# Performance work log

Hardware: AMD Instinct MI355X
Metric: run time of the kernel (lower is better)

## Reference

```python
import jax, jax.numpy as jnp
import numpy as np

ML, KS, L = 3, 7, 7  # mL, kernelSize, L = 2*mL+1


def _conv(img, kern, pad, groups=1):
    # img: [N,C,H,W], kern: [O, C//groups, kh, kw]
    return jax.lax.conv_general_dilated(
        img, kern, (1, 1), [(pad, pad), (pad, pad)],
        dimension_numbers=("NCHW", "OIHW", "NCHW"),
        feature_group_count=groups)


def setup_inputs() -> dict:
    key = jax.random.key(0)
    ks = jax.random.split(key, 16)
    B, MU = 64, 256
    lin = lambda k, fi, fo: (jax.random.normal(k, (fi, fo), jnp.float32) / np.sqrt(fi)).astype(jnp.float32)
    return {
        "x": jax.random.normal(ks[0], (B, 1, MU, MU), jnp.float32),
        "f": jax.random.normal(ks[1], (B, 1, MU, MU), jnp.float32),
        "kernelA": jax.random.normal(ks[2], (B, 1, 3, 3), jnp.float32),
        "fc1_w1": lin(ks[3], 9, 200), "fc1_b1": jnp.zeros((200,), jnp.float32),
        "fc1_w2": lin(ks[4], 200, ML * KS * KS), "fc1_b2": jnp.zeros((ML * KS * KS,), jnp.float32),
        "fc2_w1": lin(ks[5], 9, 200), "fc2_b1": jnp.zeros((200,), jnp.float32),
        "fc2_w2": lin(ks[6], 200, ML * ML * KS * KS), "fc2_b2": jnp.zeros((ML * ML * KS * KS,), jnp.float32),
    }


def reference(x, f, kernelA, fc1_w1, fc1_b1, fc1_w2, fc1_b2, fc2_w1, fc2_b1, fc2_w2, fc2_b2):
    B, _, mu, _ = x.shape
    pad = KS // 2

    # residual r = f - A x   (per-sample 3x3 stencil conv, grouped)
    r = f - jax.vmap(lambda xi, ki: _conv(xi[None], ki[None], 1)[0])(x, kernelA)  # [B,1,mu,mu]

    # meta-MLPs produce per-sample dynamic conv kernels from the 3x3 stencil
    kA = kernelA.reshape(B, 9)
    h1 = jax.nn.relu(kA @ fc1_w1 + fc1_b1)
    w1 = (h1 @ fc1_w2 + fc1_b2).reshape(B, ML, 1, KS, KS)
    h2 = jax.nn.relu(kA @ fc2_w1 + fc2_b1)
    w2 = (h2 @ fc2_w2 + fc2_b2).reshape(B, ML, ML, KS, KS)

    # per-sample dynamic convs (batched via vmap)
    G1 = jax.vmap(lambda ri, wi: _conv(ri[None], wi, pad)[0])(r, w1)    # [B,mL,mu,mu]
    G2 = jax.vmap(lambda gi, wi: _conv(gi[None], wi, pad)[0])(G1, w2)   # [B,mL,mu,mu]
    G = jnp.concatenate([r, G1, G2], axis=1)                            # [B,L,mu,mu]

    # S = A G : apply per-sample stencil to each of the L channels (depthwise)
    S = jax.vmap(lambda gi, ki: _conv(gi[None], jnp.broadcast_to(ki[None], (L, 1, 3, 3)), 1, groups=L)[0])(G, kernelA)
    S = S.reshape(B, L, mu * mu)
    Gf = G.reshape(B, L, mu * mu)
    lr = r.reshape(B, mu * mu, 1)

    # normal equations: (S S^T) K = S r, tiny [L,L] solve per sample
    M = jnp.einsum("bln,bmn->blm", S, S)    # [B,L,L]
    b = jnp.matmul(S, lr)                   # [B,L,1]
    K = jnp.linalg.solve(M, b)              # [B,L,1]

    x_new = x + jnp.matmul(K.transpose(0, 2, 1), Gf).reshape(B, 1, mu, mu)
    return x_new
```

## Files before the change

kernel.cpp:

```cpp
#include <hip/hip_runtime.h>

#define MU 256
#define NPIX (MU*MU)
#define ML 3
#define KS 7
#define LCH 7
#define NENT 35
#define RBLK 64

__global__ void mlp_kernel(const float* __restrict__ kernelA,
                           const float* __restrict__ fc1_w1, const float* __restrict__ fc1_b1,
                           const float* __restrict__ fc1_w2, const float* __restrict__ fc1_b2,
                           const float* __restrict__ fc2_w1, const float* __restrict__ fc2_b1,
                           const float* __restrict__ fc2_w2, const float* __restrict__ fc2_b2,
                           float* __restrict__ w1_out, float* __restrict__ w2_out) {
    int b = blockIdx.x;
    int t = threadIdx.x;
    __shared__ float kA[9];
    __shared__ float h1[200], h2[200];
    if (t < 9) kA[t] = kernelA[b*9 + t];
    __syncthreads();
    if (t < 200) {
        float s1 = fc1_b1[t], s2 = fc2_b1[t];
        #pragma unroll
        for (int i = 0; i < 9; ++i) {
            s1 += kA[i] * fc1_w1[i*200 + t];
            s2 += kA[i] * fc2_w1[i*200 + t];
        }
        h1[t] = fmaxf(s1, 0.f);
        h2[t] = fmaxf(s2, 0.f);
    }
    __syncthreads();
    if (t < 147) {
        float s = fc1_b2[t];
        for (int i = 0; i < 200; ++i) s += h1[i] * fc1_w2[i*147 + t];
        w1_out[b*147 + t] = s;
    }
    for (int o = t; o < 441; o += 256) {
        float s = fc2_b2[o];
        for (int i = 0; i < 200; ++i) s += h2[i] * fc2_w2[i*441 + o];
        w2_out[b*441 + o] = s;
    }
}

__global__ __launch_bounds__(256, 4) void residual_kernel(
        const float* __restrict__ x, const float* __restrict__ f,
        const float* __restrict__ kA, float* __restrict__ r) {
    int b = blockIdx.z;
    __shared__ float tile[18][72];
    int tx = threadIdx.x, ty = threadIdx.y;
    int tid = ty*64 + tx;
    float k[9];
    #pragma unroll
    for (int i = 0; i < 9; ++i) k[i] = kA[b*9 + i];
    int x0 = blockIdx.x*64, ysub = blockIdx.y*16;
    const float* xb = x + (size_t)b*NPIX;

    for (int u = tid; u < 18*18; u += 256) {
        int row = u / 18, q4 = u % 18;
        int yy = ysub + row - 1;
        int xx = x0 - 4 + q4*4;
        float4 vv = make_float4(0.f, 0.f, 0.f, 0.f);
        if (yy >= 0 && yy < MU && xx >= 0 && xx < MU)
            vv = *(const float4*)(xb + yy*MU + xx);
        *(float4*)&tile[row][q4*4] = vv;
    }
    __syncthreads();

    int ry = ty*4;
    float S0 = 0.f, S1 = 0.f, S2 = 0.f, S3 = 0.f;
    #pragma unroll
    for (int t = 0; t < 6; ++t) {
        float v0 = tile[ry + t][tx + 3];
        float v1 = tile[ry + t][tx + 4];
        float v2 = tile[ry + t][tx + 5];
        float e0 = v0*k[0] + v1*k[1] + v2*k[2];
        float e1 = v0*k[3] + v1*k[4] + v2*k[5];
        float e2 = v0*k[6] + v1*k[7] + v2*k[8];
        if (t == 0) { S0 += e0; }
        if (t == 1) { S1 += e0; S0 += e1; }
        if (t == 2) { S2 += e0; S1 += e1; S0 += e2; }
        if (t == 3) { S3 += e0; S2 += e1; S1 += e2; }
        if (t == 4) {           S3 += e1; S2 += e2; }
        if (t == 5) {                     S3 += e2; }
    }
    float Sv[4] = {S0, S1, S2, S3};
    #pragma unroll
    for (int dy = 0; dy < 4; ++dy) {
        size_t p = (size_t)b*NPIX + (size_t)(ysub + ry + dy)*MU + x0 + tx;
        r[p] = f[p] - Sv[dy];
    }
}

__global__ __launch_bounds__(256) void conv7_g1(
        const float* __restrict__ r, const float* __restrict__ w1,
        float* __restrict__ G1) {
    int b = blockIdx.z;
    __shared__ float tile[22][136];
    int tx = threadIdx.x;
    int ty = threadIdx.y;
    int tid = ty*64 + tx;
    int x0 = blockIdx.x*128, y0 = blockIdx.y*16;
    const float* rb = r + (size_t)b*NPIX;
    const float* wgt = w1 + (size_t)b*147;

    for (int u = tid; u < 22*34; u += 256) {
        int row = u / 34, q4 = u % 34;
        int yy = y0 + row - 3;
        int xx = x0 - 4 + q4*4;
        float4 vv = make_float4(0.f, 0.f, 0.f, 0.f);
        if (yy >= 0 && yy < MU && xx >= 0 && xx < MU)
            vv = *(const float4*)(rb + yy*MU + xx);
        *(float4*)&tile[row][q4*4] = vv;
    }
    __syncthreads();

    float accA[3][4], accB[3][4];
    #pragma unroll
    for (int co = 0; co < 3; ++co)
        #pragma unroll
        for (int dy = 0; dy < 4; ++dy) { accA[co][dy] = 0.f; accB[co][dy] = 0.f; }

    int ry = ty*4;
    #pragma unroll
    for (int ir = 0; ir < 10; ++ir) {
        float v[10];
        #pragma unroll
        for (int h = 0; h < 5; ++h)
            *(float2*)&v[h*2] = *(float2*)&tile[ry + ir][2*tx + h*2];
        #pragma unroll
        for (int dy = 0; dy < 4; ++dy) {
            int i = ir - dy;
            if (i >= 0 && i <= 6) {
                #pragma unroll
                for (int co = 0; co < 3; ++co)
                    #pragma unroll
                    for (int j = 0; j < 7; ++j) {
                        float w = wgt[(co*7 + i)*7 + j];
                        accA[co][dy] += v[1 + j] * w;
                        accB[co][dy] += v[2 + j] * w;
                    }
            }
        }
    }
    #pragma unroll
    for (int dy = 0; dy < 4; ++dy) {
        size_t p = (size_t)b*3*NPIX + (size_t)(y0 + ry + dy)*MU + x0 + 2*tx;
        #pragma unroll
        for (int co = 0; co < 3; ++co)
            *(float2*)&G1[p + (size_t)co*NPIX] = make_float2(accA[co][dy], accB[co][dy]);
    }
}

__global__ __launch_bounds__(256) void conv7_g2(
        const float* __restrict__ G1, const float* __restrict__ w2,
        float* __restrict__ G2) {
    int b = blockIdx.z;
    __shared__ float tile[3][14][136];
    int tx = threadIdx.x;
    int ty = threadIdx.y;
    int tid = ty*64 + tx;
    int x0 = blockIdx.x*128, y0 = blockIdx.y*8;
    const float* g1b = G1 + (size_t)b*3*NPIX;
    const float* wgt = w2 + (size_t)b*441;

    for (int u = tid; u < 3*14*34; u += 256) {
        int c = u / (14*34);
        int rem = u % (14*34);
        int row = rem / 34, q4 = rem % 34;
        int yy = y0 + row - 3;
        int xx = x0 - 4 + q4*4;
        float4 vv = make_float4(0.f, 0.f, 0.f, 0.f);
        if (yy >= 0 && yy < MU && xx >= 0 && xx < MU)
            vv = *(const float4*)(g1b + (size_t)c*NPIX + yy*MU + xx);
        *(float4*)&tile[c][row][q4*4] = vv;
    }
    __syncthreads();

    float accA[3][2], accB[3][2];
    #pragma unroll
    for (int co = 0; co < 3; ++co)
        #pragma unroll
        for (int dy = 0; dy < 2; ++dy) { accA[co][dy] = 0.f; accB[co][dy] = 0.f; }

    int ry = ty*2;
    #pragma unroll
    for (int c = 0; c < 3; ++c) {
        #pragma unroll
        for (int ir = 0; ir < 8; ++ir) {
            float v[10];
            #pragma unroll
            for (int h = 0; h < 5; ++h)
                *(float2*)&v[h*2] = *(float2*)&tile[c][ry + ir][2*tx + h*2];
            #pragma unroll
            for (int dy = 0; dy < 2; ++dy) {
                int i = ir - dy;
                if (i >= 0 && i <= 6) {
                    #pragma unroll
                    for (int co = 0; co < 3; ++co)
                        #pragma unroll
                        for (int j = 0; j < 7; ++j) {
                            float w = wgt[((co*3 + c)*7 + i)*7 + j];
                            accA[co][dy] += v[1 + j] * w;
                            accB[co][dy] += v[2 + j] * w;
                        }
                }
            }
        }
    }
    #pragma unroll
    for (int dy = 0; dy < 2; ++dy) {
        size_t p = (size_t)b*3*NPIX + (size_t)(y0 + ry + dy)*MU + x0 + 2*tx;
        #pragma unroll
        for (int co = 0; co < 3; ++co)
            *(float2*)&G2[p + (size_t)co*NPIX] = make_float2(accA[co][dy], accB[co][dy]);
    }
}

__global__ __launch_bounds__(256, 4) void reduce_kernel(
        const float* __restrict__ r, const float* __restrict__ G1,
        const float* __restrict__ G2, const float* __restrict__ kA,
        float* __restrict__ partial) {
    int b = blockIdx.z;
    __shared__ float tile[7][18][72];
    __shared__ float wsum[NENT][4];
    int tx = threadIdx.x;
    int ty = threadIdx.y;
    int tid = ty*64 + tx;
    float k[9];
    #pragma unroll
    for (int i = 0; i < 9; ++i) k[i] = kA[b*9 + i];

    const float* srcs[7] = {
        r  + (size_t)b*NPIX,
        G1 + (size_t)b*3*NPIX, G1 + (size_t)b*3*NPIX + NPIX, G1 + (size_t)b*3*NPIX + 2*NPIX,
        G2 + (size_t)b*3*NPIX, G2 + (size_t)b*3*NPIX + NPIX, G2 + (size_t)b*3*NPIX + 2*NPIX
    };

    int x0 = blockIdx.x*64;
    int ysub = blockIdx.y*16;

    #pragma unroll
    for (int c = 0; c < 7; ++c) {
        const float* src = srcs[c];
        for (int u = tid; u < 18*18; u += 256) {
            int row = u / 18, q4 = u % 18;
            int yy = ysub + row - 1;
            int xx = x0 - 4 + q4*4;
            float4 vv = make_float4(0.f, 0.f, 0.f, 0.f);
            if (yy >= 0 && yy < MU && xx >= 0 && xx < MU)
                vv = *(const float4*)(src + yy*MU + xx);
            *(float4*)&tile[c][row][q4*4] = vv;
        }
    }
    __syncthreads();

    float acc[64];
    #pragma unroll
    for (int e = 0; e < 64; ++e) acc[e] = 0.f;

    int ry = ty*4;
    float S_all[7][4];
    #pragma unroll
    for (int c = 0; c < 7; ++c) {
        float S0 = 0.f, S1 = 0.f, S2 = 0.f, S3 = 0.f;
        #pragma unroll
        for (int t = 0; t < 6; ++t) {
            float v0 = tile[c][ry + t][tx + 3];
            float v1 = tile[c][ry + t][tx + 4];
            float v2 = tile[c][ry + t][tx + 5];
            float e0 = v0*k[0] + v1*k[1] + v2*k[2];
            float e1 = v0*k[3] + v1*k[4] + v2*k[5];
            float e2 = v0*k[6] + v1*k[7] + v2*k[8];
            if (t == 0) { S0 += e0; }
            if (t == 1) { S1 += e0; S0 += e1; }
            if (t == 2) { S2 += e0; S1 += e1; S0 += e2; }
            if (t == 3) { S3 += e0; S2 += e1; S1 += e2; }
            if (t == 4) {           S3 += e1; S2 += e2; }
            if (t == 5) {                     S3 += e2; }
        }
        S_all[c][0] = S0; S_all[c][1] = S1; S_all[c][2] = S2; S_all[c][3] = S3;
    }
    #pragma unroll
    for (int dy = 0; dy < 4; ++dy) {
        float rv = tile[0][ry + dy + 1][tx + 4];
        int idx = 0;
        #pragma unroll
        for (int l = 0; l < 7; ++l) {
            #pragma unroll
            for (int m = l; m < 7; ++m) {
                acc[idx] += S_all[l][dy] * S_all[m][dy];
                ++idx;
            }
        }
        #pragma unroll
        for (int l = 0; l < 7; ++l) acc[28 + l] += S_all[l][dy] * rv;
    }

    #pragma unroll
    for (int step = 0; step < 6; ++step) {
        const int mask = 1 << step;
        const int nh = 32 >> step;
        bool hi = (tx & mask) != 0;
        #pragma unroll
        for (int i = 0; i < nh; ++i) {
            float send = hi ? acc[i] : acc[i + nh];
            float got = __shfl_xor(send, mask);
            acc[i] = (hi ? acc[i + nh] : acc[i]) + got;
        }
    }
    int ent = ((tx&1)<<5) | ((tx&2)<<3) | ((tx&4)<<1)
            | ((tx&8)>>1) | ((tx&16)>>3) | ((tx&32)>>5);
    if (ent < NENT) wsum[ent][ty] = acc[0];
    __syncthreads();
    if (tid < NENT) {
        float s = wsum[tid][0] + wsum[tid][1] + wsum[tid][2] + wsum[tid][3];
        int blockLinear = blockIdx.y*4 + blockIdx.x;
        partial[((size_t)b*NENT + tid)*RBLK + blockLinear] = s;
    }
}

__global__ void reduce2_kernel(const float* __restrict__ partial,
                               double* __restrict__ M, double* __restrict__ bv) {
    int b = blockIdx.x;
    int wave = threadIdx.x >> 6;
    int lane = threadIdx.x & 63;
    for (int e = wave; e < NENT; e += 4) {
        const float* p = partial + ((size_t)b*NENT + e)*RBLK;
        double s = (double)p[lane];
        #pragma unroll
        for (int off = 32; off; off >>= 1) s += __shfl_down(s, off);
        if (lane == 0) {
            if (e < 28) M[b*28 + e] = s;
            else        bv[b*7 + (e - 28)] = s;
        }
    }
}

__global__ __launch_bounds__(64, 1) void solve_kernel(
        const double* __restrict__ M, const double* __restrict__ bv,
        float* __restrict__ K, int B) {
    int b = blockIdx.x*64 + threadIdx.x;
    if (b >= B) return;
    double A[7][8];
    int idx = 0;
    #pragma unroll
    for (int l = 0; l < 7; ++l)
        #pragma unroll
        for (int m = l; m < 7; ++m) {
            double v = M[b*28 + idx];
            A[l][m] = v;
            A[m][l] = v;
            ++idx;
        }
    #pragma unroll
    for (int l = 0; l < 7; ++l) A[l][7] = bv[b*7 + l];

    #pragma unroll
    for (int col = 0; col < 7; ++col) {
        int piv = col;
        double mx = fabs(A[col][col]);
        #pragma unroll
        for (int rr = 0; rr < 7; ++rr) {
            if (rr > col) {
                double a = fabs(A[rr][col]);
                if (a > mx) { mx = a; piv = rr; }
            }
        }
        #pragma unroll
        for (int rr = 0; rr < 7; ++rr) {
            if (rr > col) {
                bool c = (rr == piv);
                #pragma unroll
                for (int cc = 0; cc < 8; ++cc) {
                    double t0 = A[col][cc], t1 = A[rr][cc];
                    A[col][cc] = c ? t1 : t0;
                    A[rr][cc]  = c ? t0 : t1;
                }
            }
        }
        double d = A[col][col];
        #pragma unroll
        for (int rr = 0; rr < 7; ++rr) {
            if (rr > col) {
                double fct = A[rr][col] / d;
                #pragma unroll
                for (int cc = 0; cc < 8; ++cc) A[rr][cc] -= fct * A[col][cc];
            }
        }
    }
    double Kv[7];
    #pragma unroll
    for (int rr = 6; rr >= 0; --rr) {
        double s = A[rr][7];
        #pragma unroll
        for (int cc = 0; cc < 7; ++cc)
            if (cc > rr) s -= A[rr][cc] * Kv[cc];
        Kv[rr] = s / A[rr][rr];
    }
    #pragma unroll
    for (int l = 0; l < 7; ++l) K[b*7 + l] = (float)Kv[l];
}

__global__ void update_kernel(const float* __restrict__ x, const float* __restrict__ r,
                              const float* __restrict__ G1, const float* __restrict__ G2,
                              const float* __restrict__ K, float* __restrict__ out) {
    int b = blockIdx.z;
    int p4 = blockIdx.x*256 + threadIdx.x;
    float k0 = K[b*7+0], k1 = K[b*7+1], k2 = K[b*7+2], k3 = K[b*7+3];
    float k4 = K[b*7+4], k5 = K[b*7+5], k6 = K[b*7+6];
    size_t q  = (size_t)b*(NPIX/4) + p4;
    size_t q3 = (size_t)b*3*(NPIX/4) + p4;
    const float4* x4  = (const float4*)x;
    const float4* r4  = (const float4*)r;
    const float4* g14 = (const float4*)G1;
    const float4* g24 = (const float4*)G2;
    float4 xv = x4[q], rv = r4[q];
    float4 a = g14[q3], bb = g14[q3 + NPIX/4], c = g14[q3 + 2*(NPIX/4)];
    float4 d = g24[q3], e  = g24[q3 + NPIX/4], g = g24[q3 + 2*(NPIX/4)];
    float4 o;
    o.x = xv.x + k0*rv.x + k1*a.x + k2*bb.x + k3*c.x + k4*d.x + k5*e.x + k6*g.x;
    o.y = xv.y + k0*rv.y + k1*a.y + k2*bb.y + k3*c.y + k4*d.y + k5*e.y + k6*g.y;
    o.z = xv.z + k0*rv.z + k1*a.z + k2*bb.z + k3*c.z + k4*d.z + k5*e.z + k6*g.z;
    o.w = xv.w + k0*rv.w + k1*a.w + k2*bb.w + k3*c.w + k4*d.w + k5*e.w + k6*g.w;
    ((float4*)out)[q] = o;
}

extern "C" void kernel_launch(void* const* d_in, const int* in_sizes, int n_in,
                              void* d_out, int out_size, void* d_ws, size_t ws_size,
                              hipStream_t stream) {
    const float* x       = (const float*)d_in[0];
    const float* f       = (const float*)d_in[1];
    const float* kernelA = (const float*)d_in[2];
    const float* fc1_w1  = (const float*)d_in[3];
    const float* fc1_b1  = (const float*)d_in[4];
    const float* fc1_w2  = (const float*)d_in[5];
    const float* fc1_b2  = (const float*)d_in[6];
    const float* fc2_w1  = (const float*)d_in[7];
    const float* fc2_b1  = (const float*)d_in[8];
    const float* fc2_w2  = (const float*)d_in[9];
    const float* fc2_b2  = (const float*)d_in[10];
    float* out = (float*)d_out;

    const int B = in_sizes[2] / 9;

    double* Mws = (double*)d_ws;
    double* bws = Mws + (size_t)B*28;
    float*  w1  = (float*)(bws + (size_t)B*7);
    float*  w2  = w1 + (size_t)B*147;
    float*  Kv  = w2 + (size_t)B*441;
    float*  r   = Kv + (size_t)B*7 + 1;
    float*  G1  = r  + (size_t)B*NPIX;
    float*  G2  = G1 + (size_t)B*3*NPIX;
    float*  partial = G2 + (size_t)B*3*NPIX;

    dim3 cblk(64, 4);
    dim3 rgrd(MU/64, MU/16, B);
    dim3 g1grd(MU/128, MU/16, B);
    dim3 g2grd(MU/128, MU/8, B);

    hipLaunchKernelGGL(mlp_kernel, dim3(B), dim3(256), 0, stream,
                       kernelA, fc1_w1, fc1_b1, fc1_w2, fc1_b2,
                       fc2_w1, fc2_b1, fc2_w2, fc2_b2, w1, w2);
    hipLaunchKernelGGL(residual_kernel, rgrd, cblk, 0, stream, x, f, kernelA, r);
    hipLaunchKernelGGL(conv7_g1, g1grd, cblk, 0, stream, r, w1, G1);
    hipLaunchKernelGGL(conv7_g2, g2grd, cblk, 0, stream, G1, w2, G2);
    hipLaunchKernelGGL(reduce_kernel, rgrd, cblk, 0, stream, r, G1, G2, kernelA, partial);
    hipLaunchKernelGGL(reduce2_kernel, dim3(B), dim3(256), 0, stream, partial, Mws, bws);
    hipLaunchKernelGGL(solve_kernel, dim3((B + 63)/64), dim3(64), 0, stream, Mws, bws, Kv, B);
    hipLaunchKernelGGL(update_kernel, dim3(NPIX/1024, 1, B), dim3(256), 0, stream,
                       x, r, G1, G2, Kv, out);
}
```

Before: 199.5 us.

## Drop LDS tiling in 7x7 convs, load directly from global with 4-wide register blocking

Both dynamic 7x7 conv kernels stop staging input tiles in shared memory and instead have each thread read float4 rows straight from global memory (via cache). Each thread now computes 4 columns by 2 rows per output channel, with a 32x8 block shape for both kernels. This removes the LDS fill, barrier and shared-memory reads, and gives more FMAs per loaded value horizontally. In exchange, vertical reuse is lower and the overlapping halo reads between threads and rows go through L1/L2, so global load traffic rises.

Measured after the change: 321.0 us. 60.9% more time.

```diff
diff --git a/kernel.cpp b/kernel.cpp
--- a/kernel.cpp
+++ b/kernel.cpp
@@ -96,40 +96,38 @@
         const float* __restrict__ r, const float* __restrict__ w1,
         float* __restrict__ G1) {
     int b = blockIdx.z;
-    __shared__ float tile[22][136];
     int tx = threadIdx.x;
     int ty = threadIdx.y;
-    int tid = ty*64 + tx;
     int x0 = blockIdx.x*128, y0 = blockIdx.y*16;
     const float* rb = r + (size_t)b*NPIX;
     const float* wgt = w1 + (size_t)b*147;
 
-    for (int u = tid; u < 22*34; u += 256) {
-        int row = u / 34, q4 = u % 34;
-        int yy = y0 + row - 3;
-        int xx = x0 - 4 + q4*4;
-        float4 vv = make_float4(0.f, 0.f, 0.f, 0.f);
-        if (yy >= 0 && yy < MU && xx >= 0 && xx < MU)
-            vv = *(const float4*)(rb + yy*MU + xx);
-        *(float4*)&tile[row][q4*4] = vv;
-    }
-    __syncthreads();
-
-    float accA[3][4], accB[3][4];
+    int col0 = x0 + 4*tx - 4;
+    int ry = y0 + 2*ty;
+
+    float acc[3][2][4];
     #pragma unroll
     for (int co = 0; co < 3; ++co)
         #pragma unroll
-        for (int dy = 0; dy < 4; ++dy) { accA[co][dy] = 0.f; accB[co][dy] = 0.f; }
-
-    int ry = ty*4;
-    #pragma unroll
-    for (int ir = 0; ir < 10; ++ir) {
-        float v[10];
-        #pragma unroll
-        for (int h = 0; h < 5; ++h)
-            *(float2*)&v[h*2] = *(float2*)&tile[ry + ir][2*tx + h*2];
-        #pragma unroll
-        for (int dy = 0; dy < 4; ++dy) {
+        for (int dy = 0; dy < 2; ++dy)
+            #pragma unroll
+            for (int cc = 0; cc < 4; ++cc) acc[co][dy][cc] = 0.f;
+
+    #pragma unroll
+    for (int ir = 0; ir < 8; ++ir) {
+        int yy = ry + ir - 3;
+        bool yok = (yy >= 0 && yy < MU);
+        float v[12];
+        #pragma unroll
+        for (int h = 0; h < 3; ++h) {
+            int xs = col0 + 4*h;
+            float4 vv = make_float4(0.f, 0.f, 0.f, 0.f);
+            if (yok && xs >= 0 && xs + 3 < MU)
+                vv = *(const float4*)(rb + yy*MU + xs);
+            v[4*h] = vv.x; v[4*h+1] = vv.y; v[4*h+2] = vv.z; v[4*h+3] = vv.w;
+        }
+        #pragma unroll
+        for (int dy = 0; dy < 2; ++dy) {
             int i = ir - dy;
             if (i >= 0 && i <= 6) {
                 #pragma unroll
@@ -137,18 +135,20 @@
                     #pragma unroll
                     for (int j = 0; j < 7; ++j) {
                         float w = wgt[(co*7 + i)*7 + j];
-                        accA[co][dy] += v[1 + j] * w;
-                        accB[co][dy] += v[2 + j] * w;
+                        #pragma unroll
+                        for (int cc = 0; cc < 4; ++cc)
+                            acc[co][dy][cc] += v[cc + j + 1] * w;
                     }
             }
         }
     }
     #pragma unroll
-    for (int dy = 0; dy < 4; ++dy) {
-        size_t p = (size_t)b*3*NPIX + (size_t)(y0 + ry + dy)*MU + x0 + 2*tx;
+    for (int dy = 0; dy < 2; ++dy) {
+        size_t p = (size_t)b*3*NPIX + (size_t)(ry + dy)*MU + x0 + 4*tx;
         #pragma unroll
         for (int co = 0; co < 3; ++co)
-            *(float2*)&G1[p + (size_t)co*NPIX] = make_float2(accA[co][dy], accB[co][dy]);
+            *(float4*)&G1[p + (size_t)co*NPIX] =
+                make_float4(acc[co][dy][0], acc[co][dy][1], acc[co][dy][2], acc[co][dy][3]);
     }
 }
 
@@ -156,42 +156,39 @@
         const float* __restrict__ G1, const float* __restrict__ w2,
         float* __restrict__ G2) {
     int b = blockIdx.z;
-    __shared__ float tile[3][14][136];
     int tx = threadIdx.x;
     int ty = threadIdx.y;
-    int tid = ty*64 + tx;
-    int x0 = blockIdx.x*128, y0 = blockIdx.y*8;
+    int x0 = blockIdx.x*128, y0 = blockIdx.y*16;
     const float* g1b = G1 + (size_t)b*3*NPIX;
     const float* wgt = w2 + (size_t)b*441;
 
-    for (int u = tid; u < 3*14*34; u += 256) {
-        int c = u / (14*34);
-        int rem = u % (14*34);
-        int row = rem / 34, q4 = rem % 34;
-        int yy = y0 + row - 3;
-        int xx = x0 - 4 + q4*4;
-        float4 vv = make_float4(0.f, 0.f, 0.f, 0.f);
-        if (yy >= 0 && yy < MU && xx >= 0 && xx < MU)
-            vv = *(const float4*)(g1b + (size_t)c*NPIX + yy*MU + xx);
-        *(float4*)&tile[c][row][q4*4] = vv;
-    }
-    __syncthreads();
-
-    float accA[3][2], accB[3][2];
+    int col0 = x0 + 4*tx - 4;
+    int ry = y0 + 2*ty;
+
+    float acc[3][2][4];
     #pragma unroll
     for (int co = 0; co < 3; ++co)
         #pragma unroll
-        for (int dy = 0; dy < 2; ++dy) { accA[co][dy] = 0.f; accB[co][dy] = 0.f; }
-
-    int ry = ty*2;
+        for (int dy = 0; dy < 2; ++dy)
+            #pragma unroll
+            for (int cc = 0; cc < 4; ++cc) acc[co][dy][cc] = 0.f;
+
     #pragma unroll
     for (int c = 0; c < 3; ++c) {
+        const float* src = g1b + (size_t)c*NPIX;
         #pragma unroll
         for (int ir = 0; ir < 8; ++ir) {
-            float v[10];
+            int yy = ry + ir - 3;
+            bool yok = (yy >= 0 && yy < MU);
+            float v[12];
             #pragma unroll
-            for (int h = 0; h < 5; ++h)
-                *(float2*)&v[h*2] = *(float2*)&tile[c][ry + ir][2*tx + h*2];
+            for (int h = 0; h < 3; ++h) {
+                int xs = col0 + 4*h;
+                float4 vv = make_float4(0.f, 0.f, 0.f, 0.f);
+                if (yok && xs >= 0 && xs + 3 < MU)
+                    vv = *(const float4*)(src + yy*MU + xs);
+                v[4*h] = vv.x; v[4*h+1] = vv.y; v[4*h+2] = vv.z; v[4*h+3] = vv.w;
+            }
             #pragma unroll
             for (int dy = 0; dy < 2; ++dy) {
                 int i = ir - dy;
@@ -201,8 +198,9 @@
                         #pragma unroll
                         for (int j = 0; j < 7; ++j) {
                             float w = wgt[((co*3 + c)*7 + i)*7 + j];
-                            accA[co][dy] += v[1 + j] * w;
-                            accB[co][dy] += v[2 + j] * w;
+                            #pragma unroll
+                            for (int cc = 0; cc < 4; ++cc)
+                                acc[co][dy][cc] += v[cc + j + 1] * w;
                         }
                 }
             }
@@ -210,10 +208,11 @@
     }
     #pragma unroll
     for (int dy = 0; dy < 2; ++dy) {
-        size_t p = (size_t)b*3*NPIX + (size_t)(y0 + ry + dy)*MU + x0 + 2*tx;
+        size_t p = (size_t)b*3*NPIX + (size_t)(ry + dy)*MU + x0 + 4*tx;
         #pragma unroll
         for (int co = 0; co < 3; ++co)
-            *(float2*)&G2[p + (size_t)co*NPIX] = make_float2(accA[co][dy], accB[co][dy]);
+            *(float4*)&G2[p + (size_t)co*NPIX] =
+                make_float4(acc[co][dy][0], acc[co][dy][1], acc[co][dy][2], acc[co][dy][3]);
     }
 }
 
@@ -456,15 +455,15 @@
 
     dim3 cblk(64, 4);
     dim3 rgrd(MU/64, MU/16, B);
-    dim3 g1grd(MU/128, MU/16, B);
-    dim3 g2grd(MU/128, MU/8, B);
+    dim3 gblk(32, 8);
+    dim3 ggrd(MU/128, MU/16, B);
 
     hipLaunchKernelGGL(mlp_kernel, dim3(B), dim3(256), 0, stream,
                        kernelA, fc1_w1, fc1_b1, fc1_w2, fc1_b2,
                        fc2_w1, fc2_b1, fc2_w2, fc2_b2, w1, w2);
     hipLaunchKernelGGL(residual_kernel, rgrd, cblk, 0, stream, x, f, kernelA, r);
-    hipLaunchKernelGGL(conv7_g1, g1grd, cblk, 0, stream, r, w1, G1);
-    hipLaunchKernelGGL(conv7_g2, g2grd, cblk, 0, stream, G1, w2, G2);
+    hipLaunchKernelGGL(conv7_g1, ggrd, gblk, 0, stream, r, w1, G1);
+    hipLaunchKernelGGL(conv7_g2, ggrd, gblk, 0, stream, G1, w2, G2);
     hipLaunchKernelGGL(reduce_kernel, rgrd, cblk, 0, stream, r, G1, G2, kernelA, partial);
     hipLaunchKernelGGL(reduce2_kernel, dim3(B), dim3(256), 0, stream, partial, Mws, bws);
     hipLaunchKernelGGL(solve_kernel, dim3((B + 63)/64), dim3(64), 0, stream, Mws, bws, Kv, B);
```
